# Optimization experiments

Hardware: AMD Instinct MI355X
Metric: run time of the kernel (lower is better)

The kernel has to match this reference:

```python
import jax, jax.numpy as jnp
import numpy as np

TEMPERATURE = 0.1
EPS_NORM = 1e-12  # torch F.normalize eps
EPS_LOSS = 1e-8


def setup_inputs() -> dict:
    key = jax.random.key(0)
    k1, k2 = jax.random.split(key)
    N, D, K = 8192, 512, 64
    features = jax.random.normal(k1, (N, D), dtype=jnp.float32)
    cluster_assignments = jax.random.randint(k2, (N,), 0, K, dtype=jnp.int64)
    return {"features": features, "cluster_assignments": cluster_assignments}


def reference(features, cluster_assignments):
    # L2 normalize rows (torch.nn.functional.normalize, p=2, dim=1)
    norm = jnp.linalg.norm(features, axis=1, keepdims=True)
    features_norm = features / jnp.maximum(norm, EPS_NORM)
    # pairwise cosine similarity scaled by temperature -> [N, N]
    sim = jnp.einsum('id,jd->ij', features_norm, features_norm) / TEMPERATURE
    exp_sim = jnp.exp(sim)
    mask = (cluster_assignments[None, :] == cluster_assignments[:, None]).astype(exp_sim.dtype)
    pos_sum = jnp.sum(exp_sim * mask, axis=1, keepdims=True)
    neg_sum = jnp.sum(exp_sim * (1.0 - mask), axis=1, keepdims=True)
    loss = -jnp.log(pos_sum / (pos_sum + neg_sum + EPS_LOSS))
    return jnp.sum(loss)  # reduction='sum'
```

## Files before the change

kernel.cpp:

```cpp
#include <hip/hip_runtime.h>
#include <hip/hip_bf16.h>
#include <stdint.h>

#define N 8192
#define D 512
#define TILE 128
#define BK 64
#define NKC (D / BK)
#define NTB (N / TILE)
#define NBLK (NTB * (NTB + 1) / 2)
#define PANEL_BYTES (TILE * D)
#define KCHUNK_BYTES (TILE * BK)

typedef long long i64;
typedef __attribute__((ext_vector_type(4))) float f32x4;

__device__ __forceinline__ void gload_lds16(const void* gp, const void* lp) {
    auto g = (const __attribute__((address_space(1))) void*)(uintptr_t)gp;
    auto l = (__attribute__((address_space(3))) void*)(uintptr_t)lp;
    __builtin_amdgcn_global_load_lds(g, l, 16, 0, 0);
}

__global__ void cc_normalize(const float* __restrict__ F, uint8_t* __restrict__ Fn2,
                             float* __restrict__ out) {
    if (blockIdx.x == 0 && threadIdx.x == 0) out[0] = 0.0f;
    const int row  = blockIdx.x * 4 + (threadIdx.x >> 6);
    const int lane = threadIdx.x & 63;
    const float* p = F + (size_t)row * D + lane * 8;
    float4 a = *(const float4*)p;
    float4 b = *(const float4*)(p + 4);
    float ss = a.x*a.x + a.y*a.y + a.z*a.z + a.w*a.w
             + b.x*b.x + b.y*b.y + b.z*b.z + b.w*b.w;
    #pragma unroll
    for (int m = 32; m; m >>= 1) ss += __shfl_xor(ss, m, 64);
    const float inv = 16.0f / fmaxf(sqrtf(ss), 1e-12f);
    int lo = 0, hi = 0;
    lo = __builtin_amdgcn_cvt_pk_fp8_f32(a.x*inv, a.y*inv, lo, false);
    lo = __builtin_amdgcn_cvt_pk_fp8_f32(a.z*inv, a.w*inv, lo, true);
    hi = __builtin_amdgcn_cvt_pk_fp8_f32(b.x*inv, b.y*inv, hi, false);
    hi = __builtin_amdgcn_cvt_pk_fp8_f32(b.z*inv, b.w*inv, hi, true);
    const size_t idx = (size_t)(row >> 7) * PANEL_BYTES + (size_t)lane * 1024 + (row & 127) * 8;
    *(int2*)(Fn2 + idx) = make_int2(lo, hi);
}

__global__ __launch_bounds__(256, 3)
void cc_gemm(const uint8_t* __restrict__ Fn2, const int* __restrict__ cl,
             float* __restrict__ Pt, float* __restrict__ Pp) {
    __shared__ __align__(16) uint8_t smem[6 * KCHUNK_BYTES];
    __shared__ int crow[TILE], ccol[TILE];
    uint8_t* As = smem;
    uint8_t* Bs = smem + 3 * KCHUNK_BYTES;
    float2 (*rsum)[TILE] = (float2 (*)[TILE])(smem);
    float2 (*csum)[TILE] = (float2 (*)[TILE])(smem + 4096);

    const int tid  = threadIdx.x;
    const int wave = tid >> 6;
    const int lane = tid & 63;

    int rem = blockIdx.x, bm = 0;
    while (rem >= NTB - bm) { rem -= NTB - bm; ++bm; }
    const int bn = bm + rem;
    const bool diag = (bm == bn);

    if (tid < TILE)            crow[tid]        = cl[bm * TILE + tid];
    else                       ccol[tid - TILE] = cl[bn * TILE + (tid - TILE)];

    const int wr = wave >> 1, wc = wave & 1;
    const int q   = lane >> 4;
    const int n15 = lane & 15;

    f32x4 acc[4][4];
    #pragma unroll
    for (int t = 0; t < 4; ++t)
        #pragma unroll
        for (int u = 0; u < 4; ++u) acc[t][u] = (f32x4)(0.0f);

    const uint8_t* Ag = Fn2 + (size_t)bm * PANEL_BYTES;
    const uint8_t* Bg = Fn2 + (size_t)bn * PANEL_BYTES;

    auto stage = [&](int kc, int buf) {
        const uint8_t* ga = Ag + kc * KCHUNK_BYTES;
        const uint8_t* gb = Bg + kc * KCHUNK_BYTES;
        #pragma unroll
        for (int i = 0; i < 2; ++i) {
            const int off = (wave * 2 + i) * 1024;
            gload_lds16(ga + off + lane * 16, As + buf * KCHUNK_BYTES + off);
            gload_lds16(gb + off + lane * 16, Bs + buf * KCHUNK_BYTES + off);
        }
    };

    stage(0, 0);
    stage(1, 1);

    #pragma unroll
    for (int kc = 0; kc < NKC; ++kc) {
        const int b = kc % 3;
        if (kc < NKC - 1)
            asm volatile("s_waitcnt vmcnt(4) lgkmcnt(0)\n\ts_barrier" ::: "memory");
        else
            asm volatile("s_waitcnt vmcnt(0) lgkmcnt(0)\n\ts_barrier" ::: "memory");
        if (kc + 2 < NKC) stage(kc + 2, (kc + 2) % 3);
        #pragma unroll
        for (int ks = 0; ks < 2; ++ks) {
            const int base = b * KCHUNK_BYTES + ks * 4096 + q * 1024 + n15 * 8;
            i64 af[4], bfr[4];
            #pragma unroll
            for (int t = 0; t < 4; ++t)
                af[t] = *(const i64*)&As[base + (wr * 64 + t * 16) * 8];
            #pragma unroll
            for (int u = 0; u < 4; ++u)
                bfr[u] = *(const i64*)&Bs[base + (wc * 64 + u * 16) * 8];
            #pragma unroll
            for (int t = 0; t < 4; ++t)
                #pragma unroll
                for (int u = 0; u < 4; ++u)
                    acc[t][u] = __builtin_amdgcn_mfma_f32_16x16x32_fp8_fp8(af[t], bfr[u], acc[t][u], 0, 0, 0);
        }
    }

    __syncthreads();

    const float SC = 0.05635527503472514f;
    int cc[4];
    #pragma unroll
    for (int u = 0; u < 4; ++u) cc[u] = ccol[wc * 64 + u * 16 + n15];

    float ra[16], rp[16];
    float ce[4] = {0.f, 0.f, 0.f, 0.f};
    float cp2[4] = {0.f, 0.f, 0.f, 0.f};

    #pragma unroll
    for (int t = 0; t < 4; ++t) {
        #pragma unroll
        for (int r = 0; r < 4; ++r) {
            const int myc = crow[wr * 64 + t * 16 + q * 4 + r];
            float te = 0.0f, tp = 0.0f;
            #pragma unroll
            for (int u = 0; u < 4; ++u) {
                const float e  = exp2f(acc[t][u][r] * SC);
                const float ep = (cc[u] == myc) ? e : 0.0f;
                te += e;  tp += ep;
                ce[u] += e;  cp2[u] += ep;
            }
            ra[t * 4 + r] = te;  rp[t * 4 + r] = tp;
        }
    }

    {
        int len = 16;
        #pragma unroll
        for (int m = 1; m <= 8; m <<= 1) {
            const int half = len >> 1;
            const bool hiL = (lane & m) != 0;
            #pragma unroll
            for (int j = 0; j < half; ++j) {
                float sa = hiL ? ra[j] : ra[j + half];
                float sp = hiL ? rp[j] : rp[j + half];
                sa = __shfl_xor(sa, m, 64);
                sp = __shfl_xor(sp, m, 64);
                ra[j] = (hiL ? ra[j + half] : ra[j]) + sa;
                rp[j] = (hiL ? rp[j + half] : rp[j]) + sp;
            }
            len = half;
        }
        const int idx = ((n15 & 1) << 3) | ((n15 & 2) << 1) | ((n15 & 4) >> 1) | ((n15 & 8) >> 3);
        const int row = wr * 64 + (idx >> 2) * 16 + q * 4 + (idx & 3);
        rsum[wc][row] = make_float2(ra[0], rp[0]);
    }

    if (!diag) {
        int len = 4;
        #pragma unroll
        for (int m = 16; m <= 32; m <<= 1) {
            const int half = len >> 1;
            const bool hiL = (lane & m) != 0;
            #pragma unroll
            for (int j = 0; j < half; ++j) {
                float se = hiL ? ce[j] : ce[j + half];
                float sp = hiL ? cp2[j] : cp2[j + half];
                se = __shfl_xor(se, m, 64);
                sp = __shfl_xor(sp, m, 64);
                ce[j] = (hiL ? ce[j + half] : ce[j]) + se;
                cp2[j] = (hiL ? cp2[j + half] : cp2[j]) + sp;
            }
            len = half;
        }
        const int u = (((lane >> 4) & 1) << 1) | ((lane >> 5) & 1);
        const int col = wc * 64 + u * 16 + n15;
        csum[wr][col] = make_float2(ce[0], cp2[0]);
    }

    __syncthreads();
    if (tid < TILE) {
        const float2 r0 = rsum[0][tid], r1 = rsum[1][tid];
        const size_t o = (size_t)bn * N + bm * TILE + tid;
        Pt[o] = r0.x + r1.x;  Pp[o] = r0.y + r1.y;
    } else if (!diag) {
        const int c = tid - TILE;
        const float2 c0 = csum[0][c], c1 = csum[1][c];
        const size_t o = (size_t)bm * N + bn * TILE + c;
        Pt[o] = c0.x + c1.x;  Pp[o] = c0.y + c1.y;
    }
}

__global__ void cc_finalize(const float* __restrict__ Pt, const float* __restrict__ Pp,
                            float* __restrict__ out) {
    __shared__ float red[4];
    const int i = blockIdx.x * 256 + threadIdx.x;
    float tv = 0.0f, pv = 0.0f;
    #pragma unroll 8
    for (int s = 0; s < NTB; ++s) {
        tv += Pt[(size_t)s * N + i];
        pv += Pp[(size_t)s * N + i];
    }
    float l = __logf(tv + 1e-8f) - __logf(pv);
    #pragma unroll
    for (int m = 32; m; m >>= 1) l += __shfl_xor(l, m, 64);
    const int wv = threadIdx.x >> 6, lane = threadIdx.x & 63;
    if (lane == 0) red[wv] = l;
    __syncthreads();
    if (threadIdx.x == 0) atomicAdd(out, red[0] + red[1] + red[2] + red[3]);
}

extern "C" void kernel_launch(void* const* d_in, const int* in_sizes, int n_in,
                              void* d_out, int out_size, void* d_ws, size_t ws_size,
                              hipStream_t stream) {
    const float* F  = (const float*)d_in[0];
    const int*   cl = (const int*)d_in[1];
    float* out = (float*)d_out;

    uint8_t* Fn2 = (uint8_t*)d_ws;
    float* Pt  = (float*)((char*)d_ws + (size_t)N * D);
    float* Pp  = Pt + (size_t)NTB * N;

    cc_normalize<<<N / 4, 256, 0, stream>>>(F, Fn2, out);
    cc_gemm<<<NBLK, 256, 0, stream>>>(Fn2, cl, Pt, Pp);
    cc_finalize<<<N / 256, 256, 0, stream>>>(Pt, Pp, out);
}
```

Baseline: 111.4 us.

## Use scaled 16x16x128 FP8 MFMA with direct global fragment loads

Replaces the 16x16x32 FP8 MFMA with the gfx950 scaled 16x16x128 f8f6f4 MFMA using unit scales, so each instruction covers four times the K depth. It also drops the LDS staging pipeline and loads operand fragments straight from global memory, relying on L1/L2 caches for reuse within the block. This removes the barriers and LDS traffic, but loses explicit prefetch overlap and issues many small 8-byte global loads, so memory latency may be exposed. The K-index mapping must match the lane layout of the new instruction for results to stay correct.

```diff
diff --git a/kernel.cpp b/kernel.cpp
--- a/kernel.cpp
+++ b/kernel.cpp
@@ -5,21 +5,13 @@
 #define N 8192
 #define D 512
 #define TILE 128
-#define BK 64
-#define NKC (D / BK)
 #define NTB (N / TILE)
 #define NBLK (NTB * (NTB + 1) / 2)
 #define PANEL_BYTES (TILE * D)
-#define KCHUNK_BYTES (TILE * BK)
 
 typedef long long i64;
 typedef __attribute__((ext_vector_type(4))) float f32x4;
-
-__device__ __forceinline__ void gload_lds16(const void* gp, const void* lp) {
-    auto g = (const __attribute__((address_space(1))) void*)(uintptr_t)gp;
-    auto l = (__attribute__((address_space(3))) void*)(uintptr_t)lp;
-    __builtin_amdgcn_global_load_lds(g, l, 16, 0, 0);
-}
+typedef __attribute__((ext_vector_type(8))) int i32x8;
 
 __global__ void cc_normalize(const float* __restrict__ F, uint8_t* __restrict__ Fn2,
                              float* __restrict__ out) {
@@ -46,12 +38,9 @@
 __global__ __launch_bounds__(256, 3)
 void cc_gemm(const uint8_t* __restrict__ Fn2, const int* __restrict__ cl,
              float* __restrict__ Pt, float* __restrict__ Pp) {
-    __shared__ __align__(16) uint8_t smem[6 * KCHUNK_BYTES];
     __shared__ int crow[TILE], ccol[TILE];
-    uint8_t* As = smem;
-    uint8_t* Bs = smem + 3 * KCHUNK_BYTES;
-    float2 (*rsum)[TILE] = (float2 (*)[TILE])(smem);
-    float2 (*csum)[TILE] = (float2 (*)[TILE])(smem + 4096);
+    __shared__ float2 rsum[2][TILE];
+    __shared__ float2 csum[2][TILE];
 
     const int tid  = threadIdx.x;
     const int wave = tid >> 6;
@@ -75,47 +64,36 @@
         #pragma unroll
         for (int u = 0; u < 4; ++u) acc[t][u] = (f32x4)(0.0f);
 
-    const uint8_t* Ag = Fn2 + (size_t)bm * PANEL_BYTES;
-    const uint8_t* Bg = Fn2 + (size_t)bn * PANEL_BYTES;
-
-    auto stage = [&](int kc, int buf) {
-        const uint8_t* ga = Ag + kc * KCHUNK_BYTES;
-        const uint8_t* gb = Bg + kc * KCHUNK_BYTES;
-        #pragma unroll
-        for (int i = 0; i < 2; ++i) {
-            const int off = (wave * 2 + i) * 1024;
-            gload_lds16(ga + off + lane * 16, As + buf * KCHUNK_BYTES + off);
-            gload_lds16(gb + off + lane * 16, Bs + buf * KCHUNK_BYTES + off);
-        }
-    };
-
-    stage(0, 0);
-    stage(1, 1);
-
-    #pragma unroll
-    for (int kc = 0; kc < NKC; ++kc) {
-        const int b = kc % 3;
-        if (kc < NKC - 1)
-            asm volatile("s_waitcnt vmcnt(4) lgkmcnt(0)\n\ts_barrier" ::: "memory");
-        else
-            asm volatile("s_waitcnt vmcnt(0) lgkmcnt(0)\n\ts_barrier" ::: "memory");
-        if (kc + 2 < NKC) stage(kc + 2, (kc + 2) % 3);
-        #pragma unroll
-        for (int ks = 0; ks < 2; ++ks) {
-            const int base = b * KCHUNK_BYTES + ks * 4096 + q * 1024 + n15 * 8;
-            i64 af[4], bfr[4];
-            #pragma unroll
-            for (int t = 0; t < 4; ++t)
-                af[t] = *(const i64*)&As[base + (wr * 64 + t * 16) * 8];
+    const int koff = (q >> 1) * 8192 + (q & 1) * 4096 + n15 * 8;
+    const uint8_t* Ag = Fn2 + (size_t)bm * PANEL_BYTES + koff + (wr * 64) * 8;
+    const uint8_t* Bg = Fn2 + (size_t)bn * PANEL_BYTES + koff + (wc * 64) * 8;
+
+    union F8 { i32x8 v; i64 d[4]; };
+
+    #pragma unroll
+    for (int c = 0; c < D / 128; ++c) {
+        F8 a[4], b[4];
+        #pragma unroll
+        for (int t = 0; t < 4; ++t) {
+            const uint8_t* pa = Ag + c * 16384 + t * 128;
+            #pragma unroll
+            for (int p = 0; p < 4; ++p) a[t].d[p] = *(const i64*)(pa + p * 1024);
+        }
+        #pragma unroll
+        for (int u = 0; u < 4; ++u) {
+            const uint8_t* pb = Bg + c * 16384 + u * 128;
+            #pragma unroll
+            for (int p = 0; p < 4; ++p) b[u].d[p] = *(const i64*)(pb + p * 1024);
+        }
+        #pragma unroll
+        for (int t = 0; t < 4; ++t)
             #pragma unroll
             for (int u = 0; u < 4; ++u)
-                bfr[u] = *(const i64*)&Bs[base + (wc * 64 + u * 16) * 8];
-            #pragma unroll
-            for (int t = 0; t < 4; ++t)
-                #pragma unroll
-                for (int u = 0; u < 4; ++u)
-                    acc[t][u] = __builtin_amdgcn_mfma_f32_16x16x32_fp8_fp8(af[t], bfr[u], acc[t][u], 0, 0, 0);
-        }
+                acc[t][u] = __builtin_amdgcn_mfma_scale_f32_16x16x128_f8f6f4(
+                    a[t].v, b[u].v, acc[t][u],
+                    0, 0,
+                    0, 0x7F7F7F7Fu,
+                    0, 0x7F7F7F7Fu);
     }
 
     __syncthreads();
```

Result: slower. 151.9 us (+36.4%).
